# Optimization experiments

Measured on AMD Instinct MI355X. Metric: run time of the kernel, lower is better.

## Reference

```python
import jax, jax.numpy as jnp
import numpy as np


def setup_inputs() -> dict:
    key = jax.random.key(0)
    ks = jax.random.split(key, 8)
    C = 256
    C8 = C // 8
    B, H, W = 8, 64, 64
    scale = 0.05
    return {
        "x": jax.random.normal(ks[0], (B, C, W, H), dtype=jnp.float32),
        "Wq": jax.random.normal(ks[1], (C8, C), dtype=jnp.float32) * scale,
        "bq": jax.random.normal(ks[2], (C8,), dtype=jnp.float32) * scale,
        "Wk": jax.random.normal(ks[3], (C8, C), dtype=jnp.float32) * scale,
        "bk": jax.random.normal(ks[4], (C8,), dtype=jnp.float32) * scale,
        "Wv": jax.random.normal(ks[5], (C, C), dtype=jnp.float32) * scale,
        "bv": jax.random.normal(ks[6], (C,), dtype=jnp.float32) * scale,
        "gamma": jax.random.normal(ks[7], (1,), dtype=jnp.float32),
    }


def reference(x, Wq, bq, Wk, bk, Wv, bv, gamma):
    B, C, W, H = x.shape
    N = W * H
    xf = x.reshape(B, C, N)  # flatten spatial dims: [B, C, N]
    # 1x1 convs == per-pixel channel matmuls
    q = jnp.einsum("oc,bcn->bno", Wq, xf) + bq  # [B, N, C/8]
    k = jnp.einsum("oc,bcn->bon", Wk, xf) + bk[None, :, None]  # [B, C/8, N]
    v = jnp.einsum("oc,bcn->bon", Wv, xf) + bv[None, :, None]  # [B, C, N]
    # unscaled QK^T softmax (dim=-1), as in the original
    attn = jax.nn.softmax(jnp.einsum("bno,bom->bnm", q, k), axis=-1)  # [B, N, N]
    # out[b,c,m] = sum_n v[b,c,n] * attn[b,m,n]
    out = jnp.einsum("bcn,bmn->bcm", v, attn).reshape(B, C, W, H)
    return gamma[0] * out + x
```

## Files before the change

### kernel.cpp

```cpp
#include <hip/hip_runtime.h>
#include <stdint.h>

#define B_ 8
#define C_ 256
#define N_ 4096

typedef __attribute__((ext_vector_type(8))) short short8;
typedef __attribute__((ext_vector_type(4))) float float4v;
typedef __attribute__((ext_vector_type(16))) float floatx16;

__device__ __forceinline__ uint16_t f2bfr(float f) {
  return (uint16_t)((__float_as_uint(f) + 0x8000u) >> 16);
}
__device__ __forceinline__ uint32_t pkbf(float lo, float hi) {
  return ((__float_as_uint(hi) + 0x8000u) & 0xffff0000u) |
         ((__float_as_uint(lo) + 0x8000u) >> 16);
}
__device__ __forceinline__ short8 ld8(const uint16_t* p) {
  union { ushort4 h[2]; short8 v; } u;
  u.h[0] = *reinterpret_cast<const ushort4*>(p);
  u.h[1] = *reinterpret_cast<const ushort4*>(p + 4);
  return u.v;
}

__global__ __launch_bounds__(256) void wconv_kernel(
    const float* __restrict__ Wq, const float* __restrict__ bq,
    const float* __restrict__ Wk, const float* __restrict__ bk,
    const float* __restrict__ Wv, const float* __restrict__ bv,
    uint16_t* __restrict__ Wc, float* __restrict__ bc)
{
  int tg = blockIdx.x * 256 + threadIdx.x;
  int idx = tg * 4;
  const float* src = (idx < 8192) ? (Wq + idx)
                   : (idx < 16384) ? (Wk + (idx - 8192))
                                   : (Wv + (idx - 16384));
  float4 wv = *reinterpret_cast<const float4*>(src);
  uint2 o;
  o.x = pkbf(wv.x, wv.y);
  o.y = pkbf(wv.z, wv.w);
  *reinterpret_cast<uint2*>(Wc + idx) = o;
  if (tg < 320) bc[tg] = (tg < 32) ? bq[tg] : (tg < 64) ? bk[tg - 32] : bv[tg - 64];
}

__global__ __launch_bounds__(512, 4) void qkv_mfma(
    const float* __restrict__ x, const uint16_t* __restrict__ Wc,
    const float* __restrict__ bc,
    uint16_t* __restrict__ Qw, uint16_t* __restrict__ Kw, uint16_t* __restrict__ Vw)
{
  __shared__ __align__(16) uint16_t xs[64][268];
  const int b = blockIdx.x & 7;
  const int tile = blockIdx.x >> 3;
  const int n0 = tile * 64;
  const int tid = threadIdx.x;
  const int nl = tid & 63, grp = tid >> 6;
  const int w = grp, l15 = tid & 15, q = (tid & 63) >> 4;
  const int nb = w & 3;

  const float* xb = x + (size_t)b * C_ * N_ + n0;
  #pragma unroll
  for (int it = 0; it < 16; ++it) {
    int c2 = it * 16 + grp * 2;
    float f0 = xb[(size_t)c2 * N_ + nl];
    float f1 = xb[(size_t)(c2 + 1) * N_ + nl];
    *reinterpret_cast<uint32_t*>(&xs[nl][c2]) = pkbf(f0, f1);
  }
  __syncthreads();

  float4v acc[10];
  #pragma unroll
  for (int i = 0; i < 10; ++i) acc[i] = (float4v){0.f, 0.f, 0.f, 0.f};

  const int ob0 = (w >> 2) * 10;
  #pragma unroll
  for (int h2 = 0; h2 < 2; ++h2) {
    short8 bx[4];
    #pragma unroll
    for (int kb = 0; kb < 4; ++kb)
      bx[kb] = ld8(&xs[nb * 16 + l15][h2 * 128 + kb * 32 + q * 8]);
    #pragma unroll
    for (int oi = 0; oi < 10; ++oi) {
      int ob = ob0 + oi;
      const uint16_t* wr = Wc + (size_t)(ob * 16 + l15) * 256 + h2 * 128 + q * 8;
      short8 aw[4];
      #pragma unroll
      for (int kb = 0; kb < 4; ++kb)
        aw[kb] = *reinterpret_cast<const short8*>(wr + kb * 32);
      #pragma unroll
      for (int kb = 0; kb < 4; ++kb)
        acc[oi] = __builtin_amdgcn_mfma_f32_16x16x32_bf16(aw[kb], bx[kb], acc[oi], 0, 0, 0);
    }
  }

  __syncthreads();
  uint16_t (*qs)[72] = reinterpret_cast<uint16_t(*)[72]>(&xs[0][0]);
  if (w < 4) {
    #pragma unroll
    for (int oi = 0; oi < 4; ++oi) {
      float4v a = acc[oi];
      const float* bb = bc + oi * 16 + q * 4;
      uint2 pk2;
      pk2.x = pkbf(a.x + bb[0], a.y + bb[1]);
      pk2.y = pkbf(a.z + bb[2], a.w + bb[3]);
      *reinterpret_cast<uint2*>(&qs[nb * 16 + l15][oi * 16 + q * 4]) = pk2;
    }
  }
  __syncthreads();
  if (tid < 256) {
    int n = tid >> 2, sub = tid & 3;
    const uint16_t* row = qs[n];
    uint4 d0 = *reinterpret_cast<const uint4*>(&row[sub * 16]);
    uint4 d1 = *reinterpret_cast<const uint4*>(&row[sub * 16 + 8]);
    size_t nn = (size_t)b * N_ + n0 + n;
    if (sub < 2) {
      uint4* dst = reinterpret_cast<uint4*>(Qw + nn * 32 + sub * 16);
      dst[0] = d0; dst[1] = d1;
    } else {
      uint4* dst = reinterpret_cast<uint4*>(Kw + nn * 32 + (sub - 2) * 16);
      dst[0] = d0; dst[1] = d1;
    }
  }
  const size_t blk = ((size_t)b * 64 + tile) * 4;
  const int half = l15 >> 3, j = l15 & 7;
  #pragma unroll
  for (int oi = 0; oi < 10; ++oi) {
    int ob = ob0 + oi;
    if (ob < 4) continue;
    float4v a = acc[oi];
    const float* bb = bc + ob * 16 + q * 4;
    int cb = ob * 16 - 64 + q * 4;
    size_t vaddr = (blk + (cb >> 6)) * 4096
                 + (size_t)(nb * 1024 + ((cb >> 5) & 1) * 512 + half * 256
                            + (cb & 31) * 8 + j);
    Vw[vaddr     ] = f2bfr(a.x + bb[0]);
    Vw[vaddr +  8] = f2bfr(a.y + bb[1]);
    Vw[vaddr + 16] = f2bfr(a.z + bb[2]);
    Vw[vaddr + 24] = f2bfr(a.w + bb[3]);
  }
}

__global__ __launch_bounds__(512, 4) void attn_mfma(
    const uint16_t* __restrict__ Qw, const uint16_t* __restrict__ Kw,
    const uint16_t* __restrict__ Vw, const float* __restrict__ x,
    const float* __restrict__ gamma, float* __restrict__ out)
{
  __shared__ __align__(16) union Smem {
    uint16_t Ps[2][64 * 76];
    float Os[128 * 69];
  } sm;
  __shared__ float Ls[64];

  const int b = blockIdx.x & 7;
  const int m0 = (blockIdx.x >> 3) * 64;
  const int tid = threadIdx.x;
  const int w = tid >> 6, lane = tid & 63;
  const int l15 = lane & 15, q = lane >> 4;
  const int l31 = lane & 31, half = lane >> 5;
  const int nb = w & 3, mbp = (w >> 2) * 2;

  const uint16_t* Kb = Kw + (size_t)b * N_ * 32 + (size_t)(nb * 16 + l15) * 32 + q * 8;
  const short8 qf0 = *reinterpret_cast<const short8*>(
      Qw + ((size_t)b * N_ + m0 + (mbp    ) * 16 + l15) * 32 + q * 8);
  const short8 qf1 = *reinterpret_cast<const short8*>(
      Qw + ((size_t)b * N_ + m0 + (mbp + 1) * 16 + l15) * 32 + q * 8);
  const uint16_t* Vb = Vw + ((size_t)b * 256 + (w >> 1)) * 4096
                     + (w & 1) * 512 + half * 256 + l31 * 8;

  floatx16 O[2];
  #pragma unroll
  for (int i = 0; i < 16; ++i) { O[0][i] = 0.f; O[1][i] = 0.f; }
  float rs0 = 0.f, rs1 = 0.f;
  const float4v zero4 = (float4v){0.f, 0.f, 0.f, 0.f};
  if (tid < 64) Ls[tid] = 0.f;

  short8 vc[4];
  #pragma unroll
  for (int ks = 0; ks < 4; ++ks)
    vc[ks] = *reinterpret_cast<const short8*>(Vb + ks * 1024);
  short8 kc = *reinterpret_cast<const short8*>(Kb + (size_t)64 * 32);
  {
    short8 kf = *reinterpret_cast<const short8*>(Kb);
    float4v s0 = __builtin_amdgcn_mfma_f32_16x16x32_bf16(kf, qf0, zero4, 0, 0, 0);
    float4v s1 = __builtin_amdgcn_mfma_f32_16x16x32_bf16(kf, qf1, zero4, 0, 0, 0);
    float p0 = __expf(s0.x), p1 = __expf(s0.y), p2 = __expf(s0.z), p3 = __expf(s0.w);
    rs0 += (p0 + p1) + (p2 + p3);
    uint2 pw; pw.x = pkbf(p0, p1); pw.y = pkbf(p2, p3);
    *reinterpret_cast<uint2*>(&sm.Ps[0][((mbp)*16 + l15) * 76 + nb * 16 + q * 4]) = pw;
    float r0 = __expf(s1.x), r1 = __expf(s1.y), r2 = __expf(s1.z), r3 = __expf(s1.w);
    rs1 += (r0 + r1) + (r2 + r3);
    uint2 rw; rw.x = pkbf(r0, r1); rw.y = pkbf(r2, r3);
    *reinterpret_cast<uint2*>(&sm.Ps[0][((mbp + 1)*16 + l15) * 76 + nb * 16 + q * 4]) = rw;
  }
  __syncthreads();

  for (int t = 0; t < 64; ++t) {
    const int buf = t & 1;

    short8 vn[4];
    if (t < 63) {
      const uint16_t* vt = Vb + (size_t)(t + 1) * 16384;
      #pragma unroll
      for (int ks = 0; ks < 4; ++ks)
        vn[ks] = *reinterpret_cast<const short8*>(vt + ks * 1024);
    }
    short8 kn;
    if (t < 62)
      kn = *reinterpret_cast<const short8*>(Kb + (size_t)(t + 2) * 64 * 32);

    if (t < 63) {
      float4v s0 = __builtin_amdgcn_mfma_f32_16x16x32_bf16(kc, qf0, zero4, 0, 0, 0);
      float4v s1 = __builtin_amdgcn_mfma_f32_16x16x32_bf16(kc, qf1, zero4, 0, 0, 0);
      float p0 = __expf(s0.x), p1 = __expf(s0.y), p2 = __expf(s0.z), p3 = __expf(s0.w);
      rs0 += (p0 + p1) + (p2 + p3);
      uint2 pw; pw.x = pkbf(p0, p1); pw.y = pkbf(p2, p3);
      *reinterpret_cast<uint2*>(&sm.Ps[buf ^ 1][((mbp)*16 + l15) * 76 + nb * 16 + q * 4]) = pw;
      float r0 = __expf(s1.x), r1 = __expf(s1.y), r2 = __expf(s1.z), r3 = __expf(s1.w);
      rs1 += (r0 + r1) + (r2 + r3);
      uint2 rw; rw.x = pkbf(r0, r1); rw.y = pkbf(r2, r3);
      *reinterpret_cast<uint2*>(&sm.Ps[buf ^ 1][((mbp + 1)*16 + l15) * 76 + nb * 16 + q * 4]) = rw;
    }

    #pragma unroll
    for (int ks = 0; ks < 4; ++ks) {
      short8 pa0 = ld8(&sm.Ps[buf][(l31     ) * 76 + ks * 16 + half * 8]);
      short8 pa1 = ld8(&sm.Ps[buf][(32 + l31) * 76 + ks * 16 + half * 8]);
      O[0] = __builtin_amdgcn_mfma_f32_32x32x16_bf16(pa0, vc[ks], O[0], 0, 0, 0);
      O[1] = __builtin_amdgcn_mfma_f32_32x32x16_bf16(pa1, vc[ks], O[1], 0, 0, 0);
    }
    __syncthreads();

    if (t < 63) {
      #pragma unroll
      for (int ks = 0; ks < 4; ++ks) vc[ks] = vn[ks];
    }
    if (t < 62) kc = kn;
  }

  rs0 += __shfl_xor(rs0, 16); rs0 += __shfl_xor(rs0, 32);
  rs1 += __shfl_xor(rs1, 16); rs1 += __shfl_xor(rs1, 32);
  if (q == 0) {
    atomicAdd(&Ls[(mbp    ) * 16 + l15], rs0);
    atomicAdd(&Ls[(mbp + 1) * 16 + l15], rs1);
  }
  __syncthreads();
  if (tid < 64) Ls[tid] = gamma[0] / Ls[tid];
  __syncthreads();

  #pragma unroll
  for (int chunk = 0; chunk < 2; ++chunk) {
    if ((w >> 2) == chunk) {
      int cl = (w & 3) * 32 + l31;
      #pragma unroll
      for (int h = 0; h < 2; ++h)
        #pragma unroll
        for (int reg = 0; reg < 16; ++reg) {
          int m = h * 32 + (reg & 3) + 8 * (reg >> 2) + 4 * half;
          sm.Os[cl * 69 + m] = O[h][reg] * Ls[m];
        }
    }
    __syncthreads();
    {
      int cl = tid >> 2, msub = tid & 3;
      int c = chunk * 128 + cl;
      size_t idx = ((size_t)b * C_ + c) * N_ + m0 + msub * 16;
      const float* os = &sm.Os[cl * 69 + msub * 16];
      #pragma unroll
      for (int i = 0; i < 4; ++i) {
        float4 xv = *reinterpret_cast<const float4*>(x + idx + i * 4);
        float4 ov;
        ov.x = os[i * 4 + 0] + xv.x;
        ov.y = os[i * 4 + 1] + xv.y;
        ov.z = os[i * 4 + 2] + xv.z;
        ov.w = os[i * 4 + 3] + xv.w;
        *reinterpret_cast<float4*>(out + idx + i * 4) = ov;
      }
    }
    __syncthreads();
  }
}

extern "C" void kernel_launch(void* const* d_in, const int* in_sizes, int n_in,
                              void* d_out, int out_size, void* d_ws, size_t ws_size,
                              hipStream_t stream) {
  const float* x     = (const float*)d_in[0];
  const float* Wq    = (const float*)d_in[1];
  const float* bq    = (const float*)d_in[2];
  const float* Wk    = (const float*)d_in[3];
  const float* bk    = (const float*)d_in[4];
  const float* Wv    = (const float*)d_in[5];
  const float* bv    = (const float*)d_in[6];
  const float* gamma = (const float*)d_in[7];
  float* out = (float*)d_out;

  uint16_t* Qw = (uint16_t*)d_ws;
  uint16_t* Kw = Qw + (size_t)B_ * N_ * 32;
  uint16_t* Vw = Kw + (size_t)B_ * N_ * 32;
  uint16_t* Wc = Vw + (size_t)B_ * C_ * N_;
  float*    bc = (float*)(Wc + 320 * 256);

  wconv_kernel<<<80, 256, 0, stream>>>(Wq, bq, Wk, bk, Wv, bv, Wc, bc);
  qkv_mfma<<<512, 512, 0, stream>>>(x, Wc, bc, Qw, Kw, Vw);
  attn_mfma<<<512, 512, 0, stream>>>(Qw, Kw, Vw, x, gamma, out);
}
```

Baseline: 226.1 us.

## Double the key tile per iteration to halve the barrier count

```diff
diff --git a/kernel.cpp b/kernel.cpp
--- a/kernel.cpp
+++ b/kernel.cpp
@@ -144,7 +144,7 @@
     const float* __restrict__ gamma, float* __restrict__ out)
 {
   __shared__ __align__(16) union Smem {
-    uint16_t Ps[2][64 * 76];
+    uint16_t Ps[2][64 * 140];
     float Os[128 * 69];
   } sm;
   __shared__ float Ls[64];
@@ -172,67 +172,91 @@
   const float4v zero4 = (float4v){0.f, 0.f, 0.f, 0.f};
   if (tid < 64) Ls[tid] = 0.f;
 
-  short8 vc[4];
-  #pragma unroll
-  for (int ks = 0; ks < 4; ++ks)
-    vc[ks] = *reinterpret_cast<const short8*>(Vb + ks * 1024);
-  short8 kc = *reinterpret_cast<const short8*>(Kb + (size_t)64 * 32);
-  {
-    short8 kf = *reinterpret_cast<const short8*>(Kb);
-    float4v s0 = __builtin_amdgcn_mfma_f32_16x16x32_bf16(kf, qf0, zero4, 0, 0, 0);
-    float4v s1 = __builtin_amdgcn_mfma_f32_16x16x32_bf16(kf, qf1, zero4, 0, 0, 0);
-    float p0 = __expf(s0.x), p1 = __expf(s0.y), p2 = __expf(s0.z), p3 = __expf(s0.w);
-    rs0 += (p0 + p1) + (p2 + p3);
-    uint2 pw; pw.x = pkbf(p0, p1); pw.y = pkbf(p2, p3);
-    *reinterpret_cast<uint2*>(&sm.Ps[0][((mbp)*16 + l15) * 76 + nb * 16 + q * 4]) = pw;
-    float r0 = __expf(s1.x), r1 = __expf(s1.y), r2 = __expf(s1.z), r3 = __expf(s1.w);
-    rs1 += (r0 + r1) + (r2 + r3);
-    uint2 rw; rw.x = pkbf(r0, r1); rw.y = pkbf(r2, r3);
-    *reinterpret_cast<uint2*>(&sm.Ps[0][((mbp + 1)*16 + l15) * 76 + nb * 16 + q * 4]) = rw;
-  }
-  __syncthreads();
-
-  for (int t = 0; t < 64; ++t) {
-    const int buf = t & 1;
-
-    short8 vn[4];
-    if (t < 63) {
-      const uint16_t* vt = Vb + (size_t)(t + 1) * 16384;
-      #pragma unroll
-      for (int ks = 0; ks < 4; ++ks)
-        vn[ks] = *reinterpret_cast<const short8*>(vt + ks * 1024);
-    }
-    short8 kn;
-    if (t < 62)
-      kn = *reinterpret_cast<const short8*>(Kb + (size_t)(t + 2) * 64 * 32);
-
-    if (t < 63) {
-      float4v s0 = __builtin_amdgcn_mfma_f32_16x16x32_bf16(kc, qf0, zero4, 0, 0, 0);
-      float4v s1 = __builtin_amdgcn_mfma_f32_16x16x32_bf16(kc, qf1, zero4, 0, 0, 0);
+  auto s_phase = [&](short8 k0, short8 k1, uint16_t* __restrict__ dst) {
+    float4v s0 = __builtin_amdgcn_mfma_f32_16x16x32_bf16(k0, qf0, zero4, 0, 0, 0);
+    float4v s1 = __builtin_amdgcn_mfma_f32_16x16x32_bf16(k0, qf1, zero4, 0, 0, 0);
+    float4v s2 = __builtin_amdgcn_mfma_f32_16x16x32_bf16(k1, qf0, zero4, 0, 0, 0);
+    float4v s3 = __builtin_amdgcn_mfma_f32_16x16x32_bf16(k1, qf1, zero4, 0, 0, 0);
+    {
       float p0 = __expf(s0.x), p1 = __expf(s0.y), p2 = __expf(s0.z), p3 = __expf(s0.w);
       rs0 += (p0 + p1) + (p2 + p3);
       uint2 pw; pw.x = pkbf(p0, p1); pw.y = pkbf(p2, p3);
-      *reinterpret_cast<uint2*>(&sm.Ps[buf ^ 1][((mbp)*16 + l15) * 76 + nb * 16 + q * 4]) = pw;
-      float r0 = __expf(s1.x), r1 = __expf(s1.y), r2 = __expf(s1.z), r3 = __expf(s1.w);
-      rs1 += (r0 + r1) + (r2 + r3);
-      uint2 rw; rw.x = pkbf(r0, r1); rw.y = pkbf(r2, r3);
-      *reinterpret_cast<uint2*>(&sm.Ps[buf ^ 1][((mbp + 1)*16 + l15) * 76 + nb * 16 + q * 4]) = rw;
-    }
+      *reinterpret_cast<uint2*>(&dst[((mbp)*16 + l15) * 140 + nb * 16 + q * 4]) = pw;
+    }
+    {
+      float p0 = __expf(s1.x), p1 = __expf(s1.y), p2 = __expf(s1.z), p3 = __expf(s1.w);
+      rs1 += (p0 + p1) + (p2 + p3);
+      uint2 pw; pw.x = pkbf(p0, p1); pw.y = pkbf(p2, p3);
+      *reinterpret_cast<uint2*>(&dst[((mbp + 1)*16 + l15) * 140 + nb * 16 + q * 4]) = pw;
+    }
+    {
+      float p0 = __expf(s2.x), p1 = __expf(s2.y), p2 = __expf(s2.z), p3 = __expf(s2.w);
+      rs0 += (p0 + p1) + (p2 + p3);
+      uint2 pw; pw.x = pkbf(p0, p1); pw.y = pkbf(p2, p3);
+      *reinterpret_cast<uint2*>(&dst[((mbp)*16 + l15) * 140 + (nb + 4) * 16 + q * 4]) = pw;
+    }
+    {
+      float p0 = __expf(s3.x), p1 = __expf(s3.y), p2 = __expf(s3.z), p3 = __expf(s3.w);
+      rs1 += (p0 + p1) + (p2 + p3);
+      uint2 pw; pw.x = pkbf(p0, p1); pw.y = pkbf(p2, p3);
+      *reinterpret_cast<uint2*>(&dst[((mbp + 1)*16 + l15) * 140 + (nb + 4) * 16 + q * 4]) = pw;
+    }
+  };
+
+  short8 vc[4];
+  #pragma unroll
+  for (int ks = 0; ks < 4; ++ks)
+    vc[ks] = *reinterpret_cast<const short8*>(Vb + ks * 1024);
+  short8 kc0 = *reinterpret_cast<const short8*>(Kb + (size_t)4096);
+  short8 kc1 = *reinterpret_cast<const short8*>(Kb + (size_t)4096 + 2048);
+  {
+    short8 k00 = *reinterpret_cast<const short8*>(Kb);
+    short8 k01 = *reinterpret_cast<const short8*>(Kb + 2048);
+    s_phase(k00, k01, &sm.Ps[0][0]);
+  }
+  __syncthreads();
+
+  for (int t = 0; t < 32; ++t) {
+    const int buf = t & 1;
+    const uint16_t* vt = Vb + (size_t)t * 32768;
+
+    short8 vp2[4];
+    #pragma unroll
+    for (int ks = 0; ks < 4; ++ks)
+      vp2[ks] = *reinterpret_cast<const short8*>(vt + 16384 + ks * 1024);
+    short8 vn[4];
+    short8 kn0, kn1;
+    if (t < 31) {
+      #pragma unroll
+      for (int ks = 0; ks < 4; ++ks)
+        vn[ks] = *reinterpret_cast<const short8*>(vt + 32768 + ks * 1024);
+      kn0 = *reinterpret_cast<const short8*>(Kb + (size_t)(t + 2) * 4096);
+      kn1 = *reinterpret_cast<const short8*>(Kb + (size_t)(t + 2) * 4096 + 2048);
+    }
+
+    if (t < 31) s_phase(kc0, kc1, &sm.Ps[buf ^ 1][0]);
 
     #pragma unroll
     for (int ks = 0; ks < 4; ++ks) {
-      short8 pa0 = ld8(&sm.Ps[buf][(l31     ) * 76 + ks * 16 + half * 8]);
-      short8 pa1 = ld8(&sm.Ps[buf][(32 + l31) * 76 + ks * 16 + half * 8]);
+      short8 pa0 = ld8(&sm.Ps[buf][(l31     ) * 140 + ks * 16 + half * 8]);
+      short8 pa1 = ld8(&sm.Ps[buf][(32 + l31) * 140 + ks * 16 + half * 8]);
       O[0] = __builtin_amdgcn_mfma_f32_32x32x16_bf16(pa0, vc[ks], O[0], 0, 0, 0);
       O[1] = __builtin_amdgcn_mfma_f32_32x32x16_bf16(pa1, vc[ks], O[1], 0, 0, 0);
     }
+    #pragma unroll
+    for (int ks = 0; ks < 4; ++ks) {
+      short8 pa0 = ld8(&sm.Ps[buf][(l31     ) * 140 + (ks + 4) * 16 + half * 8]);
+      short8 pa1 = ld8(&sm.Ps[buf][(32 + l31) * 140 + (ks + 4) * 16 + half * 8]);
+      O[0] = __builtin_amdgcn_mfma_f32_32x32x16_bf16(pa0, vp2[ks], O[0], 0, 0, 0);
+      O[1] = __builtin_amdgcn_mfma_f32_32x32x16_bf16(pa1, vp2[ks], O[1], 0, 0, 0);
+    }
     __syncthreads();
 
-    if (t < 63) {
+    if (t < 31) {
       #pragma unroll
       for (int ks = 0; ks < 4; ++ks) vc[ks] = vn[ks];
-    }
-    if (t < 62) kc = kn;
+      kc0 = kn0; kc1 = kn1;
+    }
   }
 
   rs0 += __shfl_xor(rs0, 16); rs0 += __shfl_xor(rs0, 32);
```

New measurement: 232.2 us. +2.7%, slower.
